# Kernel tuning notes

Measured on AMD Instinct MI355X. Metric: run time of the kernel, lower is better.

## Reference

```python
import math
import jax, jax.numpy as jnp
import numpy as np
from jax import lax

LEAKY_SLOPE = 0.2
ACT_GAIN = math.sqrt(2.0)

def bilinear_filter():
    h = jnp.array([1.0, 3.0, 3.0, 1.0], dtype=jnp.float32)
    h = h[:, None] * h[None, :]
    return h / jnp.sum(h)

def setup_inputs() -> dict:
    key = jax.random.key(0)
    ks = jax.random.split(key, 6)
    B, Cin, Cout, W_DIM, R = 16, 512, 512, 512, 64
    return {
        "x": jax.random.normal(ks[0], (B, Cin, R // 2, R // 2), dtype=jnp.float32),
        "w": jax.random.normal(ks[1], (B, W_DIM), dtype=jnp.float32),
        "noise_raw": jax.random.normal(ks[2], (B, 1, R, R), dtype=jnp.float32),
        "affine_weight": jax.random.normal(ks[3], (Cin, W_DIM), dtype=jnp.float32),
        "affine_bias": jnp.ones((Cin,), dtype=jnp.float32),
        "weight": jax.random.normal(ks[4], (Cout, Cin, 3, 3), dtype=jnp.float32),
        "bias": 0.1 * jax.random.normal(ks[5], (Cout,), dtype=jnp.float32),
        "noise_strength": jnp.float32(1.0),
    }

def reference(x, w, noise_raw, affine_weight, affine_bias, weight, bias, noise_strength):
    B, Cin = x.shape[0], x.shape[1]
    Cout = weight.shape[0]
    w_dim = affine_weight.shape[1]
    # EqualizedLinear affine: weight_gain = 1/sqrt(in), bias_gain = 1, no activation
    styles = w @ (affine_weight * (1.0 / math.sqrt(w_dim))).T + affine_bias  # [B, Cin]
    # demodulation coefficients from modulated weights
    wmod = weight[None] * styles[:, None, :, None, None]                      # [B,Cout,Cin,3,3]
    dcoefs = lax.rsqrt(jnp.sum(jnp.square(wmod), axis=(2, 3, 4)) + 1e-8)     # [B, Cout]
    # modulate input instead of weights
    xs = x * styles[:, :, None, None]
    # up=True path: conv_transpose2d(x, weight.transpose(0,1), stride=2, padding=0)
    # == dilated conv with spatially flipped kernel, pad k-1=2
    w_flip = weight[:, :, ::-1, ::-1]
    y = lax.conv_general_dilated(
        xs, w_flip, window_strides=(1, 1), padding=[(2, 2), (2, 2)],
        lhs_dilation=(2, 2), dimension_numbers=("NCHW", "OIHW", "NCHW"))    # [B,Cout,2H+1,2H+1]
    # filter2d with 4x4 bilinear kernel, gain=4, padding=1 (depthwise)
    f = bilinear_filter() * 4.0
    kd = jnp.tile(f[None, None], (Cout, 1, 1, 1))                            # [Cout,1,4,4]
    y = lax.conv_general_dilated(
        y, kd, window_strides=(1, 1), padding=[(1, 1), (1, 1)],
        dimension_numbers=("NCHW", "OIHW", "NCHW"), feature_group_count=Cout)  # [B,Cout,2H,2H]
    # addcmul: noise + y * dcoefs
    noise = noise_raw * noise_strength
    y = noise + y * dcoefs[:, :, None, None]
    # bias, act gain sqrt(2), leaky relu 0.2
    y = (y + bias[None, :, None, None]) * ACT_GAIN
    return jnp.where(y >= 0, y, LEAKY_SLOPE * y)
```

## Files before the change

kernel.cpp:

```cpp
#include <hip/hip_runtime.h>
#include <hip/hip_bf16.h>
#include <stdint.h>

typedef float f32x4 __attribute__((ext_vector_type(4)));
typedef __bf16 bf16x8 __attribute__((ext_vector_type(8)));

#define GLDS16(gp, lp) __builtin_amdgcn_global_load_lds( \
    (const __attribute__((address_space(1))) void*)(gp), \
    (__attribute__((address_space(3))) void*)(lp), 16, 0, 0)

static __device__ __forceinline__ unsigned short f2bf(float f) {
    unsigned int u = __float_as_uint(f);
    u = (u + 0x7fffu + ((u >> 16) & 1u)) >> 16;
    return (unsigned short)u;
}
static __device__ __forceinline__ float bf2f(unsigned short v) {
    return __uint_as_float(((unsigned int)v) << 16);
}

#define O_STYLES 0
#define O_DCOEF  32768
#define O_XS     65536
#define O_WP     19005440
#define O_Y1     23724032
#define O_WSQ    23724032
#define WS_NEED  96075776
#define SP 1104

__global__ __launch_bounds__(256) void k_styles(const float* __restrict__ w,
                                                const float* __restrict__ aw,
                                                const float* __restrict__ ab,
                                                float* __restrict__ styles) {
    int g = blockIdx.x * 256 + threadIdx.x;
    int b = g >> 9, ci = g & 511;
    const float4* wr = (const float4*)(w + b * 512);
    const float4* ar = (const float4*)(aw + ci * 512);
    float acc = 0.f;
    for (int k = 0; k < 128; ++k) {
        float4 wv = wr[k], av = ar[k];
        acc += wv.x * av.x + wv.y * av.y + wv.z * av.z + wv.w * av.w;
    }
    styles[g] = acc * 0.04419417382415922f + ab[ci];
}

__global__ __launch_bounds__(256) void k_wprep(const float* __restrict__ weight,
                                               float* __restrict__ wsq,
                                               unsigned short* __restrict__ wp) {
    int g = blockIdx.x * 256 + threadIdx.x;
    const float* wb = weight + (long)g * 9;
    float v[9]; float s = 0.f;
#pragma unroll
    for (int t = 0; t < 9; ++t) { v[t] = wb[t]; s += v[t] * v[t]; }
    wsq[g] = s;
    const int wri[9] = {2, 2, 0, 0, 2, 0, 1, 1, 1};
    const int wci[9] = {2, 0, 2, 0, 1, 1, 2, 0, 1};
#pragma unroll
    for (int t = 0; t < 9; ++t)
        wp[t * 262144 + g] = f2bf(v[wri[t] * 3 + wci[t]]);
}

__global__ __launch_bounds__(256) void k_dcoef(const float* __restrict__ styles,
                                               const float* __restrict__ wsq,
                                               float* __restrict__ dcoefs) {
    int g = blockIdx.x * 256 + threadIdx.x;
    int b = g >> 9, co = g & 511;
    const float4* sr = (const float4*)(styles + b * 512);
    const float4* qr = (const float4*)(wsq + co * 512);
    float acc = 1e-8f;
    for (int k = 0; k < 128; ++k) {
        float4 sv = sr[k], qv = qr[k];
        acc += sv.x * sv.x * qv.x + sv.y * sv.y * qv.y + sv.z * sv.z * qv.z + sv.w * sv.w * qv.w;
    }
    dcoefs[g] = rsqrtf(acc);
}

__global__ __launch_bounds__(256) void k_xprep(const float* __restrict__ x,
                                               const float* __restrict__ styles,
                                               unsigned short* __restrict__ xs) {
    __shared__ float T[128][33];
    int bid = blockIdx.x;
    int cc = bid & 3, i = (bid >> 2) & 31, b = bid >> 7;
    int t = threadIdx.x;
    int ci0 = cc * 128;
    int j_r = t & 31, cl_r = t >> 5;
    const float* xp = x + (((long)(b * 512 + ci0)) * 32 + i) * 32;
#pragma unroll
    for (int it = 0; it < 16; ++it) {
        int cl = cl_r + it * 8;
        T[cl][j_r] = xp[cl * 1024 + j_r];
    }
    __syncthreads();
    int ci_w = t & 127, jg = t >> 7;
    float sv = styles[b * 512 + ci0 + ci_w];
    unsigned short* op = xs + (((long)(b * 34 + (i + 1))) * 34 + 1) * 512 + ci0 + ci_w;
#pragma unroll
    for (int jj = 0; jj < 16; ++jj) {
        int j = jg * 16 + jj;
        op[(long)j * 512] = f2bf(T[ci_w][j] * sv);
    }
}

#define ST_A(kk) { GLDS16(xsB + sA0 + akt + (kk)*64, smp + nb + (kk)*16384 + t16); \
                   GLDS16(xsB + sA1 + akt + (kk)*64, smp + nb + (kk)*16384 + t16 + 8192); }
#define ST_B(kk) { GLDS16(wpB + sB0 + bkt + (kk)*64, smp + nb + 32768 + (kk)*16384 + t16); \
                   GLDS16(wpB + sB1 + bkt + (kk)*64, smp + nb + 32768 + (kk)*16384 + t16 + 8192); }
#define PHASE2(kk, STG, TAILBAR) { \
  _Pragma("unroll") for (int i = 0; i < 8; ++i) \
    av[i] = *(const bf16x8*)(smp + cb + (kk)*16384 + abase + (i*16)*64); \
  _Pragma("unroll") for (int j = 0; j < 4; ++j) \
    bv[j] = *(const bf16x8*)(smp + cb + (kk)*16384 + bbase + (j*16)*64); \
  STG; \
  __builtin_amdgcn_sched_barrier(0); \
  asm volatile("s_waitcnt vmcnt(4)" ::: "memory"); \
  __builtin_amdgcn_s_barrier(); \
  asm volatile("s_waitcnt lgkmcnt(0)" ::: "memory"); \
  __builtin_amdgcn_sched_barrier(0); \
  __builtin_amdgcn_s_setprio(1); \
  _Pragma("unroll") for (int i = 0; i < 8; ++i) \
    _Pragma("unroll") for (int j = 0; j < 4; ++j) \
      acc[i][j] = __builtin_amdgcn_mfma_f32_16x16x32_bf16(av[i], bv[j], acc[i][j], 0, 0, 0); \
  __builtin_amdgcn_s_setprio(0); \
  if (TAILBAR) __builtin_amdgcn_s_barrier(); }

__global__ __launch_bounds__(512, 2) void k_conv(const unsigned short* __restrict__ xs,
                                                 const unsigned short* __restrict__ wp,
                                                 unsigned short* __restrict__ y1) {
    extern __shared__ __align__(16) char smem[];
    const unsigned char* xsB = (const unsigned char*)xs;
    const unsigned char* wpB = (const unsigned char*)wp;
    char* smp = smem;

    int bid = blockIdx.x;
    int par, q;
    if (bid < 138)      { par = 0; q = bid; }
    else if (bid < 276) { par = 1; q = bid - 138; }
    else if (bid < 414) { par = 2; q = bid - 276; }
    else                { par = 3; q = bid - 414; }
    int Mtile = q >> 1, Ntile = q & 1;
    int a_par = par >> 1, c_par = par & 1;
    int ntaps = a_par ? (c_par ? 1 : 2) : (c_par ? 2 : 4);
    int tapofs = (par == 0) ? 0 : ((par == 1) ? 4 : ((par == 2) ? 6 : 8));
    int NKT = ntaps << 3;

    int tid = threadIdx.x;
    int lane = tid & 63, wave = tid >> 6;
    int wm = wave >> 2, wn = wave & 3;
    int lrow = lane & 15;
    int rchunk = (((lane >> 4) ^ ((lrow >> 1) & 3)) << 4);
    int abase = (wm * 128 + lrow) * 64 + rchunk;
    int bbase = 32768 + (wn * 64 + lrow) * 64 + rchunk;

    int srow = tid >> 2;
    int schunk = (((tid & 3) ^ ((tid >> 3) & 3)) << 4);
    int sA0, sA1;
    {
        unsigned gm = (unsigned)(Mtile * 256 + srow);
        if (gm > 17471u) gm = 17471u;
        unsigned b_ = gm / 1092u; unsigned pix = gm - b_ * 1092u;
        unsigned r = pix / 33u; unsigned s = pix - r * 33u;
        sA0 = (int)(((b_ * 34u + r) * 34u + s) << 10) + schunk;
        gm = (unsigned)(Mtile * 256 + srow + 128);
        if (gm > 17471u) gm = 17471u;
        b_ = gm / 1092u; pix = gm - b_ * 1092u;
        r = pix / 33u; s = pix - r * 33u;
        sA1 = (int)(((b_ * 34u + r) * 34u + s) << 10) + schunk;
    }
    int sB0 = ((Ntile * 256 + srow) << 10) + schunk;
    int sB1 = sB0 + (128 << 10);
    int t16 = tid << 4;

    f32x4 acc[8][4];
#pragma unroll
    for (int i = 0; i < 8; ++i)
#pragma unroll
        for (int j = 0; j < 4; ++j)
            acc[i][j] = (f32x4){0.f, 0.f, 0.f, 0.f};
    bf16x8 av[8], bv[4];

    auto mkA = [&](int kt) -> int {
        int tl = kt >> 3; if (tl >= ntaps) tl = ntaps - 1;
        int cib = kt & 7;
        int dio = a_par ? 1 : (c_par ? tl : (tl >> 1));
        int djo = c_par ? 1 : (a_par ? tl : (tl & 1));
        return dio * 34816 + djo * 1024 + cib * 128;
    };
    auto mkB = [&](int kt) -> long {
        int tl = kt >> 3; if (tl >= ntaps) tl = ntaps - 1;
        return (long)(tapofs + tl) * 524288 + (long)((kt & 7) * 128);
    };

    {
        int akt = mkA(0); long bkt = mkB(0); int nb = 0;
        ST_A(0); ST_B(0); ST_A(1); ST_B(1);
    }
    __builtin_amdgcn_sched_barrier(0);
    asm volatile("s_waitcnt vmcnt(4)" ::: "memory");
    __builtin_amdgcn_s_barrier();

    int cur = 0;
    for (int kt = 0; kt < NKT; ++kt) {
        int akt = mkA(kt + 1);
        long bkt = mkB(kt + 1);
        int nb = (cur ^ 1) << 16;
        int cb = cur << 16;
        PHASE2(0, { ST_A(0); ST_B(0); }, 0)
        PHASE2(1, { ST_A(1); ST_B(1); }, 1)
        cur ^= 1;
    }

#pragma unroll
    for (int mf = 0; mf < 8; ++mf) {
        int gm0 = Mtile * 256 + wm * 128 + mf * 16 + ((lane >> 4) << 2);
        if (gm0 < 17472) {
            unsigned ug = (unsigned)gm0;
            unsigned bb = ug / 1092u;
            int pix0 = (int)(ug - bb * 1092u);
            long rowb = ((long)((bb * 4u + par) * 512) + 0) * SP;
#pragma unroll
            for (int nf = 0; nf < 4; ++nf) {
                int co = Ntile * 256 + wn * 64 + nf * 16 + lrow;
                ushort4 pk;
                pk.x = f2bf(acc[mf][nf][0]);
                pk.y = f2bf(acc[mf][nf][1]);
                pk.z = f2bf(acc[mf][nf][2]);
                pk.w = f2bf(acc[mf][nf][3]);
                *(ushort4*)(y1 + rowb + (long)co * SP + pix0) = pk;
            }
        }
    }
}

__global__ __launch_bounds__(256) void k_blur(const unsigned short* __restrict__ y1,
                                              const float* __restrict__ dcoefs,
                                              const float* __restrict__ bias,
                                              const float* __restrict__ noise,
                                              const float* __restrict__ nstr,
                                              float* __restrict__ out) {
    __shared__ float yl[67 * 69];
    int bid = blockIdx.x;
    int cg = bid & 63, b = bid >> 6;
    int t = threadIdx.x;
    int n = t & 63, mq = t >> 6;
    float ns = nstr[0];

    for (int i = t; i < 67 * 69; i += 256) yl[i] = 0.f;
    __syncthreads();

    const int Rv[4] = {33, 33, 32, 32};
    const int Sv[4] = {33, 32, 33, 32};
    const float* npb = noise + b * 4096;

    for (int cc = 0; cc < 8; ++cc) {
        int co = cg * 8 + cc;
#pragma unroll
        for (int pl = 0; pl < 4; ++pl) {
            int ap = pl >> 1, cq = pl & 1;
            const unsigned short* src = y1 + ((long)((b * 4 + pl) * 512 + co)) * SP;
            int rv = Rv[pl], sv = Sv[pl];
            for (int it = t; it < 273; it += 256) {
                int p0 = it * 4;
                ushort4 v = *(const ushort4*)(src + p0);
                unsigned short vv[4] = {v.x, v.y, v.z, v.w};
#pragma unroll
                for (int k = 0; k < 4; ++k) {
                    int p = p0 + k;
                    if (p < 1089) {
                        int r = p / 33;
                        int s = p - r * 33;
                        if (r < rv && s < sv)
                            yl[(2 * r + ap + 1) * 69 + (2 * s + cq + 1)] = bf2f(vv[k]);
                    }
                }
            }
        }
        __syncthreads();

        float dc = dcoefs[b * 512 + co];
        float bi = bias[co];
        int m0 = mq * 16;
        const float* r0p = &yl[(m0 - 1 + 1) * 69 + n];
        const float* r1p = r0p + 69;
        const float* r2p = r1p + 69;
        float t0 = (r0p[0] + r0p[3]) + 3.f * (r0p[1] + r0p[2]);
        float t1 = (r1p[0] + r1p[3]) + 3.f * (r1p[1] + r1p[2]);
        float t2 = (r2p[0] + r2p[3]) + 3.f * (r2p[1] + r2p[2]);
        float* ob = out + ((long)(b * 512 + co)) * 4096;
#pragma unroll
        for (int k = 0; k < 16; ++k) {
            int m = m0 + k;
            const float* rp = &yl[(m + 3) * 69 + n];
            float t3 = (rp[0] + rp[3]) + 3.f * (rp[1] + rp[2]);
            float a = (t0 + t3) + 3.f * (t1 + t2);
            float val = npb[m * 64 + n] * ns + a * (0.0625f * dc);
            val = (val + bi) * 1.41421356237309515f;
            ob[m * 64 + n] = (val >= 0.f) ? val : 0.2f * val;
            t0 = t1; t1 = t2; t2 = t3;
        }
        __syncthreads();
    }
}

extern "C" void kernel_launch(void* const* d_in, const int* in_sizes, int n_in,
                              void* d_out, int out_size, void* d_ws, size_t ws_size,
                              hipStream_t stream) {
    (void)in_sizes; (void)n_in; (void)out_size;
    if (ws_size < (size_t)WS_NEED) return;
    const float* x      = (const float*)d_in[0];
    const float* w      = (const float*)d_in[1];
    const float* noise  = (const float*)d_in[2];
    const float* aw     = (const float*)d_in[3];
    const float* ab     = (const float*)d_in[4];
    const float* weight = (const float*)d_in[5];
    const float* bias   = (const float*)d_in[6];
    const float* nstr   = (const float*)d_in[7];
    float* out = (float*)d_out;
    char* ws = (char*)d_ws;
    float* styles          = (float*)(ws + O_STYLES);
    float* dcoefs          = (float*)(ws + O_DCOEF);
    unsigned short* xs     = (unsigned short*)(ws + O_XS);
    unsigned short* wp     = (unsigned short*)(ws + O_WP);
    unsigned short* y1     = (unsigned short*)(ws + O_Y1);
    float* wsq             = (float*)(ws + O_WSQ);

    hipFuncSetAttribute((const void*)k_conv,
                        hipFuncAttributeMaxDynamicSharedMemorySize, 131072);

    hipMemsetAsync(xs, 0, 18939904, stream);
    k_styles<<<32,   256, 0, stream>>>(w, aw, ab, styles);
    k_wprep <<<1024, 256, 0, stream>>>(weight, wsq, wp);
    k_dcoef <<<32,   256, 0, stream>>>(styles, wsq, dcoefs);
    k_xprep <<<2048, 256, 0, stream>>>(x, styles, xs);
    k_conv  <<<552,  512, 131072, stream>>>(xs, wp, y1);
    k_blur  <<<1024, 256, 0, stream>>>(y1, dcoefs, bias, noise, nstr, out);
}
```

Measured before the change: 212.6 us.

## Split heavy parity conv work into extra blocks and restructure blur per parity plane

When the workspace is large enough, the parity-0 conv job, which has four taps, is split into two two-tap jobs written to separate planes. This gives 690 balanced blocks instead of 552 unbalanced ones, and the blur sums the two partial planes. The blur kernel now keeps the four parity planes in separate compact LDS tiles and applies the 4x4 filter as parity-aware separable weights, with half the channels per block and twice the blocks. The staging loads are also issued before the LDS fragment reads. The cost is an extra plane of bf16 intermediate traffic plus a second read in the blur, and the faster path only runs when the workspace is at least 113 MB.

```diff
diff --git a/kernel.cpp b/kernel.cpp
--- a/kernel.cpp
+++ b/kernel.cpp
@@ -24,8 +24,8 @@
 #define O_WP     19005440
 #define O_Y1     23724032
 #define O_WSQ    23724032
-#define WS_NEED  96075776
-#define SP 1104
+#define WS_NEED4 96075776
+#define WS_NEED5 113180672
 
 __global__ __launch_bounds__(256) void k_styles(const float* __restrict__ w,
                                                 const float* __restrict__ aw,
@@ -105,11 +105,11 @@
 #define ST_B(kk) { GLDS16(wpB + sB0 + bkt + (kk)*64, smp + nb + 32768 + (kk)*16384 + t16); \
                    GLDS16(wpB + sB1 + bkt + (kk)*64, smp + nb + 32768 + (kk)*16384 + t16 + 8192); }
 #define PHASE2(kk, STG, TAILBAR) { \
+  STG; \
   _Pragma("unroll") for (int i = 0; i < 8; ++i) \
     av[i] = *(const bf16x8*)(smp + cb + (kk)*16384 + abase + (i*16)*64); \
   _Pragma("unroll") for (int j = 0; j < 4; ++j) \
     bv[j] = *(const bf16x8*)(smp + cb + (kk)*16384 + bbase + (j*16)*64); \
-  STG; \
   __builtin_amdgcn_sched_barrier(0); \
   asm volatile("s_waitcnt vmcnt(4)" ::: "memory"); \
   __builtin_amdgcn_s_barrier(); \
@@ -124,22 +124,33 @@
 
 __global__ __launch_bounds__(512, 2) void k_conv(const unsigned short* __restrict__ xs,
                                                  const unsigned short* __restrict__ wp,
-                                                 unsigned short* __restrict__ y1) {
+                                                 unsigned short* __restrict__ y1,
+                                                 int mode, int sp, int npl) {
     extern __shared__ __align__(16) char smem[];
     const unsigned char* xsB = (const unsigned char*)xs;
     const unsigned char* wpB = (const unsigned char*)wp;
     char* smp = smem;
 
     int bid = blockIdx.x;
-    int par, q;
-    if (bid < 138)      { par = 0; q = bid; }
-    else if (bid < 276) { par = 1; q = bid - 138; }
-    else if (bid < 414) { par = 2; q = bid - 276; }
-    else                { par = 3; q = bid - 414; }
+    int par, tbase, ntaps, plane, q;
+    if (mode) {
+        int jt = bid / 138; q = bid - jt * 138;
+        const int parj[5]   = {0, 0, 1, 2, 3};
+        const int tbasej[5] = {0, 2, 0, 0, 0};
+        const int ntj[5]    = {2, 2, 2, 2, 1};
+        par = parj[jt]; tbase = tbasej[jt]; ntaps = ntj[jt]; plane = jt;
+    } else {
+        if (bid < 138)      { par = 0; q = bid; }
+        else if (bid < 276) { par = 1; q = bid - 138; }
+        else if (bid < 414) { par = 2; q = bid - 276; }
+        else                { par = 3; q = bid - 414; }
+        tbase = 0;
+        ntaps = (par == 0) ? 4 : ((par == 3) ? 1 : 2);
+        plane = par;
+    }
     int Mtile = q >> 1, Ntile = q & 1;
     int a_par = par >> 1, c_par = par & 1;
-    int ntaps = a_par ? (c_par ? 1 : 2) : (c_par ? 2 : 4);
-    int tapofs = (par == 0) ? 0 : ((par == 1) ? 4 : ((par == 2) ? 6 : 8));
+    const int parbase = (par == 0) ? 0 : ((par == 1) ? 4 : ((par == 2) ? 6 : 8));
     int NKT = ntaps << 3;
 
     int tid = threadIdx.x;
@@ -177,16 +188,19 @@
             acc[i][j] = (f32x4){0.f, 0.f, 0.f, 0.f};
     bf16x8 av[8], bv[4];
 
+    auto tlf = [&](int kt) -> int {
+        int tl = kt >> 3; int c = ntaps - 1; if (tl > c) tl = c;
+        return tbase + tl;
+    };
     auto mkA = [&](int kt) -> int {
-        int tl = kt >> 3; if (tl >= ntaps) tl = ntaps - 1;
+        int tl = tlf(kt);
         int cib = kt & 7;
         int dio = a_par ? 1 : (c_par ? tl : (tl >> 1));
         int djo = c_par ? 1 : (a_par ? tl : (tl & 1));
         return dio * 34816 + djo * 1024 + cib * 128;
     };
     auto mkB = [&](int kt) -> long {
-        int tl = kt >> 3; if (tl >= ntaps) tl = ntaps - 1;
-        return (long)(tapofs + tl) * 524288 + (long)((kt & 7) * 128);
+        return (long)(parbase + tlf(kt)) * 524288 + (long)((kt & 7) * 128);
     };
 
     {
@@ -215,16 +229,23 @@
             unsigned ug = (unsigned)gm0;
             unsigned bb = ug / 1092u;
             int pix0 = (int)(ug - bb * 1092u);
-            long rowb = ((long)((bb * 4u + par) * 512) + 0) * SP;
+            unsigned rr = (unsigned)pix0 % 33u;
+            long rowb = ((long)(bb * npl + plane) * 512) * sp;
 #pragma unroll
             for (int nf = 0; nf < 4; ++nf) {
                 int co = Ntile * 256 + wn * 64 + nf * 16 + lrow;
-                ushort4 pk;
-                pk.x = f2bf(acc[mf][nf][0]);
-                pk.y = f2bf(acc[mf][nf][1]);
-                pk.z = f2bf(acc[mf][nf][2]);
-                pk.w = f2bf(acc[mf][nf][3]);
-                *(ushort4*)(y1 + rowb + (long)co * SP + pix0) = pk;
+                if (pix0 <= 1084) {
+                    ushort4 pk;
+                    pk.x = f2bf(acc[mf][nf][0]);
+                    pk.y = f2bf(acc[mf][nf][1]);
+                    pk.z = f2bf(acc[mf][nf][2]);
+                    pk.w = f2bf(acc[mf][nf][3]);
+                    if (c_par && rr >= 29)
+                        ((unsigned short*)&pk)[32 - rr] = 0;
+                    *(ushort4*)(y1 + rowb + (long)co * sp + pix0) = pk;
+                } else if (pix0 == 1088) {
+                    y1[rowb + (long)co * sp + 1088] = c_par ? (unsigned short)0 : f2bf(acc[mf][nf][0]);
+                }
             }
         }
     }
@@ -235,40 +256,54 @@
                                               const float* __restrict__ bias,
                                               const float* __restrict__ noise,
                                               const float* __restrict__ nstr,
-                                              float* __restrict__ out) {
-    __shared__ float yl[67 * 69];
+                                              float* __restrict__ out,
+                                              int mode, int sp, int npl) {
+    __shared__ float yl[4 * 35 * 36];
     int bid = blockIdx.x;
-    int cg = bid & 63, b = bid >> 6;
+    int cg = bid & 127, b = bid >> 7;
     int t = threadIdx.x;
     int n = t & 63, mq = t >> 6;
     float ns = nstr[0];
 
-    for (int i = t; i < 67 * 69; i += 256) yl[i] = 0.f;
+    for (int i = t; i < 5040; i += 256) yl[i] = 0.f;
     __syncthreads();
 
-    const int Rv[4] = {33, 33, 32, 32};
-    const int Sv[4] = {33, 32, 33, 32};
+    const int rvv[4] = {33, 33, 32, 32};
+    const int ps5[4] = {0, 2, 3, 4};
     const float* npb = noise + b * 4096;
 
-    for (int cc = 0; cc < 8; ++cc) {
-        int co = cg * 8 + cc;
+    int o = n & 1;
+    int se = n >> 1;
+    int sp_ = se - 1 + o;
+    float a0 = o ? 1.f : 3.f;
+    float a1 = o ? 3.f : 1.f;
+
+    for (int cc = 0; cc < 4; ++cc) {
+        int co = cg * 4 + cc;
 #pragma unroll
         for (int pl = 0; pl < 4; ++pl) {
-            int ap = pl >> 1, cq = pl & 1;
-            const unsigned short* src = y1 + ((long)((b * 4 + pl) * 512 + co)) * SP;
-            int rv = Rv[pl], sv = Sv[pl];
+            int ps = mode ? ps5[pl] : pl;
+            int pc = (mode && pl == 0) ? 2 : 1;
+            const unsigned short* s0 = y1 + ((long)(b * npl + ps) * 512 + co) * sp;
+            float* dst = yl + pl * 1260;
+            int pv = rvv[pl] * 33;
+            long pstr = (long)512 * sp;
             for (int it = t; it < 273; it += 256) {
                 int p0 = it * 4;
-                ushort4 v = *(const ushort4*)(src + p0);
-                unsigned short vv[4] = {v.x, v.y, v.z, v.w};
+                ushort4 v = *(const ushort4*)(s0 + p0);
+                float f0 = bf2f(v.x), f1 = bf2f(v.y), f2 = bf2f(v.z), f3 = bf2f(v.w);
+                if (pc == 2) {
+                    ushort4 w2 = *(const ushort4*)(s0 + pstr + p0);
+                    f0 += bf2f(w2.x); f1 += bf2f(w2.y); f2 += bf2f(w2.z); f3 += bf2f(w2.w);
+                }
+                float ff[4] = {f0, f1, f2, f3};
 #pragma unroll
                 for (int k = 0; k < 4; ++k) {
                     int p = p0 + k;
-                    if (p < 1089) {
-                        int r = p / 33;
-                        int s = p - r * 33;
-                        if (r < rv && s < sv)
-                            yl[(2 * r + ap + 1) * 69 + (2 * s + cq + 1)] = bf2f(vv[k]);
+                    if (p < pv && p < 1089) {
+                        unsigned r = (unsigned)p / 33u;
+                        unsigned s = (unsigned)p - r * 33u;
+                        dst[(r + 1) * 36 + (s + 1)] = ff[k];
                     }
                 }
             }
@@ -277,24 +312,34 @@
 
         float dc = dcoefs[b * 512 + co];
         float bi = bias[co];
+        float* ob = out + ((long)(b * 512 + co)) * 4096;
+
+        auto H = [&](int ap, int r) -> float {
+            const float* pe = yl + (ap * 2) * 1260 + (r + 1) * 36;
+            const float* po = pe + 1260;
+            return a0 * pe[se + 1] + a1 * pe[se + 2] + a1 * po[sp_ + 1] + a0 * po[sp_ + 2];
+        };
+
         int m0 = mq * 16;
-        const float* r0p = &yl[(m0 - 1 + 1) * 69 + n];
-        const float* r1p = r0p + 69;
-        const float* r2p = r1p + 69;
-        float t0 = (r0p[0] + r0p[3]) + 3.f * (r0p[1] + r0p[2]);
-        float t1 = (r1p[0] + r1p[3]) + 3.f * (r1p[1] + r1p[2]);
-        float t2 = (r2p[0] + r2p[3]) + 3.f * (r2p[1] + r2p[2]);
-        float* ob = out + ((long)(b * 512 + co)) * 4096;
-#pragma unroll
-        for (int k = 0; k < 16; ++k) {
+        int re = m0 >> 1;
+        float he0 = H(0, re), he1 = H(0, re + 1);
+        float ho0 = H(1, re - 1), ho1 = H(1, re);
+#pragma unroll
+        for (int k = 0; k < 16; k += 2) {
             int m = m0 + k;
-            const float* rp = &yl[(m + 3) * 69 + n];
-            float t3 = (rp[0] + rp[3]) + 3.f * (rp[1] + rp[2]);
-            float a = (t0 + t3) + 3.f * (t1 + t2);
-            float val = npb[m * 64 + n] * ns + a * (0.0625f * dc);
+            float ve = 3.f * he0 + he1 + ho0 + 3.f * ho1;
+            float val = npb[m * 64 + n] * ns + ve * (0.0625f * dc);
             val = (val + bi) * 1.41421356237309515f;
             ob[m * 64 + n] = (val >= 0.f) ? val : 0.2f * val;
-            t0 = t1; t1 = t2; t2 = t3;
+            float hn_o = H(1, re + 1);
+            float vo = he0 + 3.f * he1 + 3.f * ho1 + hn_o;
+            val = npb[(m + 1) * 64 + n] * ns + vo * (0.0625f * dc);
+            val = (val + bi) * 1.41421356237309515f;
+            ob[(m + 1) * 64 + n] = (val >= 0.f) ? val : 0.2f * val;
+            ho0 = ho1; ho1 = hn_o;
+            float hn_e = H(0, re + 2);
+            he0 = he1; he1 = hn_e;
+            re += 1;
         }
         __syncthreads();
     }
@@ -304,7 +349,12 @@
                               void* d_out, int out_size, void* d_ws, size_t ws_size,
                               hipStream_t stream) {
     (void)in_sizes; (void)n_in; (void)out_size;
-    if (ws_size < (size_t)WS_NEED) return;
+    if (ws_size < (size_t)WS_NEED4) return;
+    int mode = (ws_size >= (size_t)WS_NEED5) ? 1 : 0;
+    int sp   = mode ? 1092 : 1104;
+    int npl  = mode ? 5 : 4;
+    int nblk = mode ? 690 : 552;
+
     const float* x      = (const float*)d_in[0];
     const float* w      = (const float*)d_in[1];
     const float* noise  = (const float*)d_in[2];
@@ -330,6 +380,6 @@
     k_wprep <<<1024, 256, 0, stream>>>(weight, wsq, wp);
     k_dcoef <<<32,   256, 0, stream>>>(styles, wsq, dcoefs);
     k_xprep <<<2048, 256, 0, stream>>>(x, styles, xs);
-    k_conv  <<<552,  512, 131072, stream>>>(xs, wp, y1);
-    k_blur  <<<1024, 256, 0, stream>>>(y1, dcoefs, bias, noise, nstr, out);
-}
+    k_conv  <<<nblk, 512, 131072, stream>>>(xs, wp, y1, mode, sp, npl);
+    k_blur  <<<2048, 256, 0, stream>>>(y1, dcoefs, bias, noise, nstr, out, mode, sp, npl);
+}
```

After: 247.6 us. 1.16x slower.
